# Kernel tuning notes

Measured on AMD Instinct MI355X. Metric: run time of the kernel, lower is better.

## Reference

```python
import jax, jax.numpy as jnp
import numpy as np

N = 800_000
D = 128
S = 64
EPS = 1e-16  # matches torch_geometric softmax denominator epsilon


def setup_inputs() -> dict:
    key = jax.random.key(0)
    k1, k2, k3 = jax.random.split(key, 3)
    x = jax.random.normal(k1, (N, D), dtype=jnp.float32)
    batch = jnp.sort(jax.random.randint(k2, (N,), 0, S, dtype=jnp.int64))
    gate_W = jax.random.normal(k3, (D, 1), dtype=jnp.float32) * (1.0 / np.sqrt(D))
    gate_b = jnp.zeros((1,), dtype=jnp.float32)
    return {"x": x, "batch": batch, "size": S, "gate_W": gate_W, "gate_b": gate_b}


def reference(x, batch, size, gate_W, gate_b):
    # gate = gate_nn(x).view(-1, 1)  -> [N]
    gate = (x @ gate_W + gate_b)[:, 0]
    # segment-wise numerically-stable softmax over nodes of each graph
    seg_max = jax.ops.segment_max(gate, batch, num_segments=size,
                                  indices_are_sorted=True)
    # guard empty segments (-inf max)
    seg_max = jnp.where(jnp.isfinite(seg_max), seg_max, 0.0)
    g = jnp.exp(gate - seg_max[batch])
    denom = jax.ops.segment_sum(g, batch, num_segments=size,
                                indices_are_sorted=True)
    gate_sm = g / (denom[batch] + EPS)          # [N]
    # weighted scatter-add pooling: out[s] = sum_{i in seg s} gate_i * x_i
    out = jax.ops.segment_sum(gate_sm[:, None] * x, batch, num_segments=size,
                              indices_are_sorted=True)  # [S, D]
    return out, gate_sm[:, None]
```

## Files before the change

### kernel.cpp

```cpp
#include <hip/hip_runtime.h>
#include <hip/hip_bf16.h>
#include <math.h>

#define D 128
#define EPS 1e-16f
#define K_SLOTS 4
#define REC_STRIDE 132
#define NBLK_A 2048
#define THR_A 256
#define NWV (NBLK_A * THR_A / 64)
#define NREC (NWV * K_SLOTS)
#define NBLK_R 256
#define RB (NREC / NBLK_R)

__device__ __forceinline__ unsigned f2o(float f) {
    unsigned u = __float_as_uint(f);
    return (u & 0x80000000u) ? ~u : (u | 0x80000000u);
}
__device__ __forceinline__ float o2f(unsigned o) {
    return (o & 0x80000000u) ? __uint_as_float(o & 0x7fffffffu) : __uint_as_float(~o);
}
__device__ __forceinline__ float bcast0(float v) {
    return __uint_as_float(__builtin_amdgcn_readfirstlane(__float_as_uint(v)));
}

__global__ void k_init(unsigned* __restrict__ segMkey, float* __restrict__ denomAcc,
                       float* __restrict__ outAcc, float* __restrict__ recs, int S) {
    const int t = blockIdx.x * blockDim.x + threadIdx.x;
    const int stride = gridDim.x * blockDim.x;
    for (int i = t; i < S; i += stride) { segMkey[i] = 0x007FFFFFu; denomAcc[i] = 0.f; }
    for (int i = t; i < S * D; i += stride) outAcc[i] = 0.f;
    for (int r = t; r < NREC; r += stride) ((int*)recs)[(size_t)r * REC_STRIDE] = -1;
}

__global__ __launch_bounds__(256) void k_fused(const float* __restrict__ x,
        const int* __restrict__ batch,
        const float* __restrict__ W,
        const float* __restrict__ bptr,
        float* __restrict__ gate,
        float* __restrict__ recs,
        unsigned* __restrict__ segMkey,
        int N, int chunk) {
    const int lane = threadIdx.x & 63;
    const int sub  = lane & 31;
    const int h    = lane >> 5;
    const int wv   = (blockIdx.x * blockDim.x + threadIdx.x) >> 6;
    const int i0   = wv * chunk;
    const int i1   = min(N, i0 + chunk);
    if (i0 >= i1) return;
    float* myrec = recs + (size_t)wv * K_SLOTS * REC_STRIDE;

    const float4 w = ((const float4*)W)[sub];
    const float bias = bptr[0];

    float4 acc = make_float4(0.f, 0.f, 0.f, 0.f);
    float m = -INFINITY, l = 0.f;
    int cur = batch[i0];
    int cnt = 0;

    auto flush = [&]() {
        acc.x += __shfl_xor(acc.x, 32);
        acc.y += __shfl_xor(acc.y, 32);
        acc.z += __shfl_xor(acc.z, 32);
        acc.w += __shfl_xor(acc.w, 32);
        float* r = myrec + min(cnt, K_SLOTS - 1) * REC_STRIDE;
        if (lane == 0) { ((int*)r)[0] = cur; r[1] = m; r[2] = l; }
        if (h == 0) ((float4*)(r + 4))[sub] = acc;
        if (lane == 0) atomicMax(&segMkey[cur], f2o(m));
        ++cnt;
        acc = make_float4(0.f, 0.f, 0.f, 0.f); m = -INFINITY; l = 0.f;
    };

    auto one = [&](int b, float gs, int hr, float4 xv) {
        if (b != cur) { flush(); cur = b; }
        const float m2 = fmaxf(m, gs);
        const float s  = __expf(m - m2);
        const float e  = __expf(gs - m2);
        l = l * s + e;
        const float es = (h == hr) ? e : 0.f;
        acc.x = acc.x * s + es * xv.x;
        acc.y = acc.y * s + es * xv.y;
        acc.z = acc.z * s + es * xv.z;
        acc.w = acc.w * s + es * xv.w;
        m = m2;
    };

    const int n = i1 - i0;
    const int npair = n >> 1;

    if (npair > 0) {
        float4 xc = ((const float4*)(x + (size_t)i0 * D))[lane];
        int b0c = batch[i0], b1c = batch[i0 + 1];
        float4 xn = xc; int b0n = b0c, b1n = b1c;
        if (npair > 1) {
            xn = ((const float4*)(x + (size_t)(i0 + 2) * D))[lane];
            b0n = batch[i0 + 2]; b1n = batch[i0 + 3];
        }
        for (int p = 0; p < npair; ++p) {
            float4 x2 = xn; int b02 = b0n, b12 = b1n;
            if (p + 2 < npair) {
                const int ir = i0 + 2 * (p + 2);
                x2 = ((const float4*)(x + (size_t)ir * D))[lane];
                b02 = batch[ir]; b12 = batch[ir + 1];
            }
            const int i = i0 + 2 * p;
            float pd = xc.x * w.x + xc.y * w.y + xc.z * w.z + xc.w * w.w;
            pd += __shfl_xor(pd, 1);
            pd += __shfl_xor(pd, 2);
            pd += __shfl_xor(pd, 4);
            pd += __shfl_xor(pd, 8);
            pd += __shfl_xor(pd, 16);
            const float g  = pd + bias;
            const float go = __shfl_xor(g, 32);
            const float g0 = bcast0(g);
            const float g1 = bcast0(go);
            if (sub == 0) gate[i + h] = g;

            if (b0c == cur && b1c == cur) {
                const float m2 = fmaxf(fmaxf(m, g0), g1);
                const float s  = __expf(m - m2);
                const float e  = __expf(g - m2);
                l = l * s + __expf(g0 - m2) + __expf(g1 - m2);
                acc.x = acc.x * s + e * xc.x;
                acc.y = acc.y * s + e * xc.y;
                acc.z = acc.z * s + e * xc.z;
                acc.w = acc.w * s + e * xc.w;
                m = m2;
            } else {
                one(b0c, g0, 0, xc);
                one(b1c, g1, 1, xc);
            }
            xc = xn; b0c = b0n; b1c = b1n;
            xn = x2; b0n = b02; b1n = b12;
        }
    }
    if (n & 1) {
        const int i = i1 - 1;
        float4 xt = ((const float4*)(x + (size_t)i * D))[sub];
        float pd = xt.x * w.x + xt.y * w.y + xt.z * w.z + xt.w * w.w;
        pd += __shfl_xor(pd, 1);
        pd += __shfl_xor(pd, 2);
        pd += __shfl_xor(pd, 4);
        pd += __shfl_xor(pd, 8);
        pd += __shfl_xor(pd, 16);
        const float gs = bcast0(pd + bias);
        if (lane == 0) gate[i] = gs;
        one(batch[i], gs, 0, xt);
    }
    flush();
}

__global__ __launch_bounds__(128) void k_acc(const float* __restrict__ recs,
        const unsigned* __restrict__ segMkey,
        float* __restrict__ denomAcc, float* __restrict__ outAcc) {
    const int j  = threadIdx.x;
    const int r0 = blockIdx.x * RB;
    float a = 0.f, dl = 0.f;
    int curseg = -1;
    for (int r = r0; r < r0 + RB; ++r) {
        const float* rec = recs + (size_t)r * REC_STRIDE;
        const int seg = ((const int*)rec)[0];
        if (seg < 0) continue;
        if (seg != curseg) {
            if (curseg >= 0) {
                atomicAdd(&outAcc[(size_t)curseg * D + j], a);
                if (j == 0) atomicAdd(&denomAcc[curseg], dl);
            }
            curseg = seg; a = 0.f; dl = 0.f;
        }
        const float sc = __expf(rec[1] - o2f(segMkey[seg]));
        a += sc * rec[4 + j];
        if (j == 0) dl += sc * rec[2];
    }
    if (curseg >= 0) {
        atomicAdd(&outAcc[(size_t)curseg * D + j], a);
        if (j == 0) atomicAdd(&denomAcc[curseg], dl);
    }
}

__global__ void k_final(const float* __restrict__ gate,
                        const int* __restrict__ batch,
                        const unsigned* __restrict__ segMkey,
                        const float* __restrict__ denomAcc,
                        const float* __restrict__ outAcc,
                        float* __restrict__ out, float* __restrict__ gate_sm,
                        int N, int SD) {
    const int t = blockIdx.x * blockDim.x + threadIdx.x;
    if (t < SD) out[t] = outAcc[t] / (denomAcc[t >> 7] + EPS);
    const int stride = gridDim.x * blockDim.x;
    for (int i = t; i < N; i += stride) {
        const int b = batch[i];
        gate_sm[i] = __expf(gate[i] - o2f(segMkey[b])) / (denomAcc[b] + EPS);
    }
}

extern "C" void kernel_launch(void* const* d_in, const int* in_sizes, int n_in,
                              void* d_out, int out_size, void* d_ws, size_t ws_size,
                              hipStream_t stream) {
    const float* x      = (const float*)d_in[0];
    const int*   batch  = (const int*)d_in[1];
    const float* gate_W = (const float*)d_in[3];
    const float* gate_b = (const float*)d_in[4];

    const int N = in_sizes[0] / D;
    const int S = (out_size - N) / D;

    float* out     = (float*)d_out;
    float* gate_sm = (float*)d_out + (size_t)S * D;

    float*    gate     = (float*)d_ws;
    unsigned* segMkey  = (unsigned*)(gate + N);
    float*    denomAcc = (float*)(segMkey + S);
    float*    outAcc   = denomAcc + S;
    size_t off = ((size_t)(N + 2 * S + S * D) + 3) & ~(size_t)3;
    float*    recs     = (float*)d_ws + off;

    int chunk = (N + NWV - 1) / NWV;
    chunk = (chunk + 1) & ~1;

    k_init<<<128, 256, 0, stream>>>(segMkey, denomAcc, outAcc, recs, S);
    k_fused<<<NBLK_A, THR_A, 0, stream>>>(x, batch, gate_W, gate_b, gate, recs, segMkey, N, chunk);
    k_acc<<<NBLK_R, 128, 0, stream>>>(recs, segMkey, denomAcc, outAcc);
    k_final<<<1024, 256, 0, stream>>>(gate, batch, segMkey, denomAcc, outAcc, out, gate_sm, N, S * D);
}
```

Baseline: 628.5 us.

## Process four rows per iteration with a uniform-segment fast path in fused gate kernel

The fused gate/online-softmax kernel now first checks whether a wave's whole chunk lies in one segment. If it does, it runs a fast path that handles four rows per iteration as two float4 loads per lane, uses readlane broadcasts, and writes the gate values as one float4 store. Chunks that cross a segment boundary fall back to a simple per-row loop, and the chunk size is rounded to a multiple of four. The aim is to cut per-row branching and shuffle overhead and to get more loads in flight, at the cost of a slower path for boundary chunks.

```diff
diff --git a/kernel.cpp b/kernel.cpp
--- a/kernel.cpp
+++ b/kernel.cpp
@@ -20,8 +20,8 @@
 __device__ __forceinline__ float o2f(unsigned o) {
     return (o & 0x80000000u) ? __uint_as_float(o & 0x7fffffffu) : __uint_as_float(~o);
 }
-__device__ __forceinline__ float bcast0(float v) {
-    return __uint_as_float(__builtin_amdgcn_readfirstlane(__float_as_uint(v)));
+__device__ __forceinline__ float rlf(float v, int l) {
+    return __uint_as_float(__builtin_amdgcn_readlane(__float_as_uint(v), l));
 }
 
 __global__ void k_init(unsigned* __restrict__ segMkey, float* __restrict__ denomAcc,
@@ -59,93 +59,87 @@
     int cnt = 0;
 
     auto flush = [&]() {
-        acc.x += __shfl_xor(acc.x, 32);
-        acc.y += __shfl_xor(acc.y, 32);
-        acc.z += __shfl_xor(acc.z, 32);
-        acc.w += __shfl_xor(acc.w, 32);
+        float4 t = acc;
+        t.x += __shfl_xor(t.x, 32);
+        t.y += __shfl_xor(t.y, 32);
+        t.z += __shfl_xor(t.z, 32);
+        t.w += __shfl_xor(t.w, 32);
         float* r = myrec + min(cnt, K_SLOTS - 1) * REC_STRIDE;
-        if (lane == 0) { ((int*)r)[0] = cur; r[1] = m; r[2] = l; }
-        if (h == 0) ((float4*)(r + 4))[sub] = acc;
-        if (lane == 0) atomicMax(&segMkey[cur], f2o(m));
+        if (lane == 0) {
+            ((int*)r)[0] = cur; r[1] = m; r[2] = l;
+            atomicMax(&segMkey[cur], f2o(m));
+        }
+        if (h == 0) ((float4*)(r + 4))[sub] = t;
         ++cnt;
         acc = make_float4(0.f, 0.f, 0.f, 0.f); m = -INFINITY; l = 0.f;
     };
 
-    auto one = [&](int b, float gs, int hr, float4 xv) {
+    auto one_row = [&](int i) {
+        const int b = batch[i];
         if (b != cur) { flush(); cur = b; }
-        const float m2 = fmaxf(m, gs);
+        float4 xv = ((const float4*)(x + (size_t)i * D))[sub];
+        float p = xv.x * w.x + xv.y * w.y + xv.z * w.z + xv.w * w.w;
+        p += __shfl_xor(p, 1);
+        p += __shfl_xor(p, 2);
+        p += __shfl_xor(p, 4);
+        p += __shfl_xor(p, 8);
+        p += __shfl_xor(p, 16);
+        const float g = p + bias;
+        if (lane == 0) gate[i] = g;
+        const float m2 = fmaxf(m, g);
         const float s  = __expf(m - m2);
-        const float e  = __expf(gs - m2);
+        const float e  = __expf(g - m2);
         l = l * s + e;
-        const float es = (h == hr) ? e : 0.f;
-        acc.x = acc.x * s + es * xv.x;
-        acc.y = acc.y * s + es * xv.y;
-        acc.z = acc.z * s + es * xv.z;
-        acc.w = acc.w * s + es * xv.w;
+        const float eh = (h == 0) ? e : 0.f;
+        acc.x = acc.x * s + eh * xv.x;
+        acc.y = acc.y * s + eh * xv.y;
+        acc.z = acc.z * s + eh * xv.z;
+        acc.w = acc.w * s + eh * xv.w;
         m = m2;
     };
 
-    const int n = i1 - i0;
-    const int npair = n >> 1;
-
-    if (npair > 0) {
-        float4 xc = ((const float4*)(x + (size_t)i0 * D))[lane];
-        int b0c = batch[i0], b1c = batch[i0 + 1];
-        float4 xn = xc; int b0n = b0c, b1n = b1c;
-        if (npair > 1) {
-            xn = ((const float4*)(x + (size_t)(i0 + 2) * D))[lane];
-            b0n = batch[i0 + 2]; b1n = batch[i0 + 3];
-        }
-        for (int p = 0; p < npair; ++p) {
-            float4 x2 = xn; int b02 = b0n, b12 = b1n;
-            if (p + 2 < npair) {
-                const int ir = i0 + 2 * (p + 2);
-                x2 = ((const float4*)(x + (size_t)ir * D))[lane];
-                b02 = batch[ir]; b12 = batch[ir + 1];
+    if (batch[i1 - 1] == cur) {
+        const int nq = (i1 - i0) >> 2;
+        const float* xp = x + (size_t)i0 * D;
+        float4 xa, xb, na, nb;
+        if (nq > 0) {
+            xa = ((const float4*)xp)[lane];
+            xb = ((const float4*)(xp + 2 * D))[lane];
+        }
+        for (int q = 0; q < nq; ++q) {
+            const float* xq = xp + 4 * D;
+            if (q + 1 < nq) {
+                na = ((const float4*)xq)[lane];
+                nb = ((const float4*)(xq + 2 * D))[lane];
             }
-            const int i = i0 + 2 * p;
-            float pd = xc.x * w.x + xc.y * w.y + xc.z * w.z + xc.w * w.w;
-            pd += __shfl_xor(pd, 1);
-            pd += __shfl_xor(pd, 2);
-            pd += __shfl_xor(pd, 4);
-            pd += __shfl_xor(pd, 8);
-            pd += __shfl_xor(pd, 16);
-            const float g  = pd + bias;
-            const float go = __shfl_xor(g, 32);
-            const float g0 = bcast0(g);
-            const float g1 = bcast0(go);
-            if (sub == 0) gate[i + h] = g;
-
-            if (b0c == cur && b1c == cur) {
-                const float m2 = fmaxf(fmaxf(m, g0), g1);
-                const float s  = __expf(m - m2);
-                const float e  = __expf(g - m2);
-                l = l * s + __expf(g0 - m2) + __expf(g1 - m2);
-                acc.x = acc.x * s + e * xc.x;
-                acc.y = acc.y * s + e * xc.y;
-                acc.z = acc.z * s + e * xc.z;
-                acc.w = acc.w * s + e * xc.w;
-                m = m2;
-            } else {
-                one(b0c, g0, 0, xc);
-                one(b1c, g1, 1, xc);
-            }
-            xc = xn; b0c = b0n; b1c = b1n;
-            xn = x2; b0n = b02; b1n = b12;
-        }
-    }
-    if (n & 1) {
-        const int i = i1 - 1;
-        float4 xt = ((const float4*)(x + (size_t)i * D))[sub];
-        float pd = xt.x * w.x + xt.y * w.y + xt.z * w.z + xt.w * w.w;
-        pd += __shfl_xor(pd, 1);
-        pd += __shfl_xor(pd, 2);
-        pd += __shfl_xor(pd, 4);
-        pd += __shfl_xor(pd, 8);
-        pd += __shfl_xor(pd, 16);
-        const float gs = bcast0(pd + bias);
-        if (lane == 0) gate[i] = gs;
-        one(batch[i], gs, 0, xt);
+            float pa = xa.x * w.x + xa.y * w.y + xa.z * w.z + xa.w * w.w;
+            float pb = xb.x * w.x + xb.y * w.y + xb.z * w.z + xb.w * w.w;
+            pa += __shfl_xor(pa, 1);  pb += __shfl_xor(pb, 1);
+            pa += __shfl_xor(pa, 2);  pb += __shfl_xor(pb, 2);
+            pa += __shfl_xor(pa, 4);  pb += __shfl_xor(pb, 4);
+            pa += __shfl_xor(pa, 8);  pb += __shfl_xor(pb, 8);
+            pa += __shfl_xor(pa, 16); pb += __shfl_xor(pb, 16);
+            const float ga = pa + bias;
+            const float gb = pb + bias;
+            const float g0 = rlf(ga, 0), g1 = rlf(ga, 32);
+            const float g2 = rlf(gb, 0), g3 = rlf(gb, 32);
+            const float m2 = fmaxf(fmaxf(fmaxf(fmaxf(m, g0), g1), g2), g3);
+            const float s  = __expf(m - m2);
+            const float ea = __expf(ga - m2);
+            const float eb = __expf(gb - m2);
+            l = l * s + ((rlf(ea, 0) + rlf(ea, 32)) + (rlf(eb, 0) + rlf(eb, 32)));
+            acc.x = (acc.x * s + ea * xa.x) + eb * xb.x;
+            acc.y = (acc.y * s + ea * xa.y) + eb * xb.y;
+            acc.z = (acc.z * s + ea * xa.z) + eb * xb.z;
+            acc.w = (acc.w * s + ea * xa.w) + eb * xb.w;
+            m = m2;
+            if (lane == 0)
+                *((float4*)(gate + i0 + 4 * q)) = make_float4(g0, g1, g2, g3);
+            xa = na; xb = nb; xp = xq;
+        }
+        for (int i = i0 + 4 * nq; i < i1; ++i) one_row(i);
+    } else {
+        for (int i = i0; i < i1; ++i) one_row(i);
     }
     flush();
 }
@@ -216,7 +210,7 @@
     float*    recs     = (float*)d_ws + off;
 
     int chunk = (N + NWV - 1) / NWV;
-    chunk = (chunk + 1) & ~1;
+    chunk = (chunk + 3) & ~3;
 
     k_init<<<128, 256, 0, stream>>>(segMkey, denomAcc, outAcc, recs, S);
     k_fused<<<NBLK_A, THR_A, 0, stream>>>(x, batch, gate_W, gate_b, gate, recs, segMkey, N, chunk);
```

After: 674.2 us. 1.07x slower.
